# Kernel tuning notes

Measured on AMD Instinct MI355X. Metric: run time of the kernel, lower is better.

Reference implementation:

```python
import jax, jax.numpy as jnp
import numpy as np

B, S = 8, 2048

def setup_inputs() -> dict:
    key = jax.random.key(0)
    ks = iter(jax.random.split(key, 64))
    def lin(din, dout):
        w = jax.random.normal(next(ks), (din, dout), jnp.float32) / np.float32(np.sqrt(din))
        b = jax.random.normal(next(ks), (dout,), jnp.float32) * 0.01
        return w, b
    inp = {}
    inp['x'] = jax.random.normal(next(ks), (B, S, 256), jnp.float32)
    def blk(tag, d, ff):
        for name, (din, dout) in [('q',(d,d)),('k',(d,d)),('v',(d,d)),('o',(d,d)),('ff1',(d,ff)),('ff2',(ff,d))]:
            w, b = lin(din, dout)
            inp[f'{name}_w{tag}'] = w; inp[f'{name}_b{tag}'] = b
        inp[f'ln1_g{tag}'] = jnp.ones((d,), jnp.float32); inp[f'ln1_b{tag}'] = jnp.zeros((d,), jnp.float32)
        inp[f'ln2_g{tag}'] = jnp.ones((d,), jnp.float32); inp[f'ln2_b{tag}'] = jnp.zeros((d,), jnp.float32)
    blk(1, 256, 1024)
    blk(2, 128, 512)
    for nm, (din, dout) in [('dr1',(256,128)),('dr2',(128,64)),('dr3',(64,32)),('dr4',(32,14))]:
        w, b = lin(din, dout)
        inp[f'{nm}_w'] = w; inp[f'{nm}_b'] = b
    return inp

def _ln(x, g, b, eps=1e-5):
    m = x.mean(-1, keepdims=True)
    v = ((x - m) ** 2).mean(-1, keepdims=True)
    return (x - m) / jnp.sqrt(v + eps) * g + b

def _mha(x, wq, bq, wk, bk, wv, bv, wo, bo, h):
    Bx, Sx, D = x.shape
    hd = D // h
    q = (x @ wq + bq).reshape(Bx, Sx, h, hd).transpose(0, 2, 1, 3)
    k = (x @ wk + bk).reshape(Bx, Sx, h, hd).transpose(0, 2, 1, 3)
    v = (x @ wv + bv).reshape(Bx, Sx, h, hd).transpose(0, 2, 1, 3)
    scores = jnp.einsum('bhqd,bhkd->bhqk', q, k) / jnp.sqrt(jnp.float32(hd))  # [B,h,S,S]
    p = jax.nn.softmax(scores, axis=-1)
    o = jnp.einsum('bhqk,bhkd->bqhd', p, v).reshape(Bx, Sx, D)
    return o @ wo + bo

def _encoder(x, p, h):
    a = _mha(x, p['qw'], p['qb'], p['kw'], p['kb'], p['vw'], p['vb'], p['ow'], p['ob'], h)
    x = _ln(a + x, p['g1'], p['b1'])
    f = jax.nn.relu(x @ p['fw1'] + p['fb1']) @ p['fw2'] + p['fb2']
    return _ln(f + x, p['g2'], p['b2'])

def _pe(s, d):
    pos = jnp.arange(s, dtype=jnp.float32)[:, None]
    dep = jnp.arange(d, dtype=jnp.float32)[None, :]
    ang = pos / jnp.power(jnp.float32(10000.0), dep / d)
    even = (jnp.arange(d)[None, :] % 2) == 0
    return jnp.where(even, jnp.sin(ang), jnp.cos(ang))

def _forward(x,
             q_w1, q_b1, k_w1, k_b1, v_w1, v_b1, o_w1, o_b1,
             ff1_w1, ff1_b1, ff2_w1, ff2_b1, ln1_g1, ln1_b1, ln2_g1, ln2_b1,
             dr1_w, dr1_b,
             q_w2, q_b2, k_w2, k_b2, v_w2, v_b2, o_w2, o_b2,
             ff1_w2, ff1_b2, ff2_w2, ff2_b2, ln1_g2, ln1_b2, ln2_g2, ln2_b2,
             dr2_w, dr2_b, dr3_w, dr3_b, dr4_w, dr4_b):
    h = x + _pe(x.shape[1], x.shape[2])
    p1 = dict(qw=q_w1, qb=q_b1, kw=k_w1, kb=k_b1, vw=v_w1, vb=v_b1, ow=o_w1, ob=o_b1,
              fw1=ff1_w1, fb1=ff1_b1, fw2=ff2_w1, fb2=ff2_b1, g1=ln1_g1, b1=ln1_b1, g2=ln2_g1, b2=ln2_b1)
    h = _encoder(h, p1, 8)
    h = h @ dr1_w + dr1_b
    p2 = dict(qw=q_w2, qb=q_b2, kw=k_w2, kb=k_b2, vw=v_w2, vb=v_b2, ow=o_w2, ob=o_b2,
              fw1=ff1_w2, fb1=ff1_b2, fw2=ff2_w2, fb2=ff2_b2, g1=ln1_g2, b1=ln1_b2, g2=ln2_g2, b2=ln2_b2)
    h = _encoder(h, p2, 8)
    h = h @ dr2_w + dr2_b
    h = jnp.max(h, axis=1)  # AdaptiveMaxPool1d(1) over the sequence dim -> [B, 64]
    h = h @ dr3_w + dr3_b
    return h @ dr4_w + dr4_b  # [B, 14]

def reference(x,
              q_w1, q_b1, k_w1, k_b1, v_w1, v_b1, o_w1, o_b1,
              ff1_w1, ff1_b1, ff2_w1, ff2_b1, ln1_g1, ln1_b1, ln2_g1, ln2_b1,
              dr1_w, dr1_b,
              q_w2, q_b2, k_w2, k_b2, v_w2, v_b2, o_w2, o_b2,
              ff1_w2, ff1_b2, ff2_w2, ff2_b2, ln1_g2, ln1_b2, ln2_g2, ln2_b2,
              dr2_w, dr2_b, dr3_w, dr3_b, dr4_w, dr4_b):
    return _forward(x,
                    q_w1, q_b1, k_w1, k_b1, v_w1, v_b1, o_w1, o_b1,
                    ff1_w1, ff1_b1, ff2_w1, ff2_b1, ln1_g1, ln1_b1, ln2_g1, ln2_b1,
                    dr1_w, dr1_b,
                    q_w2, q_b2, k_w2, k_b2, v_w2, v_b2, o_w2, o_b2,
                    ff1_w2, ff1_b2, ff2_w2, ff2_b2, ln1_g2, ln1_b2, ln2_g2, ln2_b2,
                    dr2_w, dr2_b, dr3_w, dr3_b, dr4_w, dr4_b)
```

## Files before the change

### kernel.cpp

```cpp
#include <hip/hip_runtime.h>
#include <hip/hip_bf16.h>
#include <math.h>

#define SEQ  2048
#define BATCH 8
#define NTOK (SEQ*BATCH)

typedef __attribute__((ext_vector_type(8))) short short8v;
typedef __attribute__((ext_vector_type(4))) float f32x4;
typedef unsigned short u16;

__device__ __forceinline__ u16 f2bf(float f) {
    __hip_bfloat16 h = __float2bfloat16(f);
    return *reinterpret_cast<u16*>(&h);
}
__device__ __forceinline__ unsigned pack_bf2(float a, float b) {
    __hip_bfloat162 h = __float22bfloat162_rn(float2{a, b});
    return *reinterpret_cast<unsigned*>(&h);
}
__device__ __forceinline__ void gl_lds16(const u16* g, u16* l) {
    __builtin_amdgcn_global_load_lds(
        (const __attribute__((address_space(1))) unsigned int*)g,
        (__attribute__((address_space(3))) unsigned int*)l, 16, 0, 0);
}

struct WDescs {
    const float* src[14];
    int K[14];
    int N[14];
    long dst[14];
    float scale[14];
    int tstart[15];
};

__global__ __launch_bounds__(256) void convert_w_kernel(WDescs d, u16* __restrict__ WA) {
    __shared__ float tile[64][65];
    int blk = blockIdx.x;
    int di = 0;
    while (di < 13 && blk >= d.tstart[di + 1]) ++di;
    int t  = blk - d.tstart[di];
    int K  = d.K[di], N = d.N[di];
    int tn = N >> 6;
    int k0 = (t / tn) << 6, n0 = (t % tn) << 6;
    const float* src = d.src[di];
    float sc = d.scale[di];
    int tid = threadIdx.x;
    #pragma unroll
    for (int i = 0; i < 16; ++i) {
        int id = i * 256 + tid;
        int kk = id >> 6, nn = id & 63;
        tile[kk][nn] = src[(size_t)(k0 + kk) * N + n0 + nn];
    }
    __syncthreads();
    u16* dst = WA + d.dst[di];
    #pragma unroll
    for (int i = 0; i < 16; ++i) {
        int id = i * 256 + tid;
        int nn = id >> 6, kk = id & 63;
        dst[(size_t)(n0 + nn) * K + k0 + kk] = f2bf(tile[kk][nn] * sc);
    }
}

__global__ __launch_bounds__(256) void convert_bias_kernel(
    const float* qb1, const float* kb1, const float* vb1,
    const float* qb2, const float* kb2, const float* vb2,
    const float* dr2b, float* __restrict__ BA, float qs1, float qs2)
{
    int t = blockIdx.x * 256 + threadIdx.x;
    if      (t < 256)  BA[t] = qb1[t] * qs1;
    else if (t < 512)  BA[t] = kb1[t - 256];
    else if (t < 768)  BA[t] = vb1[t - 512];
    else if (t < 896)  BA[t] = qb2[t - 768] * qs2;
    else if (t < 1024) BA[t] = kb2[t - 896];
    else if (t < 1152) BA[t] = vb2[t - 1024];
    else if (t < 1216) BA[t] = dr2b[t - 1152];
    else if (t < 1280) BA[t] = 0.f;
}

__global__ __launch_bounds__(256) void add_pe_kernel(const float* __restrict__ x,
                                                     float* __restrict__ h,
                                                     u16* __restrict__ hb) {
    int idx = blockIdx.x * 256 + threadIdx.x;
    int s = idx >> 8;
    int d = idx & 255;
    float inv = exp2f((float)d * -0.0519051264732f);
    float ang = (float)s * inv;
    float pe  = (d & 1) ? __cosf(ang) : __sinf(ang);
    #pragma unroll
    for (int b = 0; b < BATCH; ++b) {
        size_t g = ((size_t)(b * SEQ + s) << 8) + d;
        float v = x[g] + pe;
        h[g]  = v;
        hb[g] = f2bf(v);
    }
}

template<int BM, int BN, int RELU, int WF32, int WBF16>
__global__ __launch_bounds__(256) void gemm_bf16_kernel(
    const u16* __restrict__ A, const u16* __restrict__ Bt,
    const float* __restrict__ bias, float* __restrict__ Cf,
    u16* __restrict__ Cb, int N, int K)
{
    constexpr int NMF = BM / 32;
    constexpr int NBF = BN / 32;
    __shared__ u16 As[BM * 64];
    __shared__ u16 Bs[BN * 64];
    const int tid  = threadIdx.x;
    const int lane = tid & 63;
    const int c    = lane & 15, g = lane >> 4;
    const int w    = tid >> 6;
    const int wr   = w >> 1, wc = w & 1;
    const size_t bm = (size_t)blockIdx.y * BM;
    const size_t bn = (size_t)blockIdx.x * BN;

    f32x4 acc[NMF][NBF];
    #pragma unroll
    for (int i = 0; i < NMF; ++i)
        #pragma unroll
        for (int j = 0; j < NBF; ++j) acc[i][j] = (f32x4){0.f, 0.f, 0.f, 0.f};

    const int nt = K >> 6;
    for (int t = 0; t < nt; ++t) {
        #pragma unroll
        for (int j = 0; j < BM / 32; ++j) {
            int cid = j * 256 + tid;
            int row = cid >> 3, blk = cid & 7;
            int sof = (blk ^ (row & 7)) * 8;
            gl_lds16(&A[(bm + row) * K + t * 64 + sof], &As[cid * 8]);
        }
        #pragma unroll
        for (int j = 0; j < BN / 32; ++j) {
            int cid = j * 256 + tid;
            int row = cid >> 3, blk = cid & 7;
            int sof = (blk ^ (row & 7)) * 8;
            gl_lds16(&Bt[(bn + row) * K + t * 64 + sof], &Bs[cid * 8]);
        }
        __syncthreads();
        #pragma unroll
        for (int ks2 = 0; ks2 < 2; ++ks2) {
            short8v af[NMF], bfr[NBF];
            #pragma unroll
            for (int am = 0; am < NMF; ++am) {
                int r = wr * (BM / 2) + am * 16 + c;
                af[am] = *(const short8v*)&As[r * 64 + (((ks2 * 4 + g) ^ (r & 7)) * 8)];
            }
            #pragma unroll
            for (int bn_ = 0; bn_ < NBF; ++bn_) {
                int r = wc * (BN / 2) + bn_ * 16 + c;
                bfr[bn_] = *(const short8v*)&Bs[r * 64 + (((ks2 * 4 + g) ^ (r & 7)) * 8)];
            }
            #pragma unroll
            for (int am = 0; am < NMF; ++am)
                #pragma unroll
                for (int bn_ = 0; bn_ < NBF; ++bn_)
                    acc[am][bn_] = __builtin_amdgcn_mfma_f32_16x16x32_bf16(
                                       af[am], bfr[bn_], acc[am][bn_], 0, 0, 0);
        }
        __syncthreads();
    }

    float bv[NBF];
    #pragma unroll
    for (int bn_ = 0; bn_ < NBF; ++bn_) bv[bn_] = bias[bn + wc * (BN / 2) + bn_ * 16 + c];
    #pragma unroll
    for (int am = 0; am < NMF; ++am) {
        #pragma unroll
        for (int bn_ = 0; bn_ < NBF; ++bn_) {
            #pragma unroll
            for (int i = 0; i < 4; ++i) {
                size_t row = bm + wr * (BM / 2) + am * 16 + 4 * g + i;
                size_t col = bn + wc * (BN / 2) + bn_ * 16 + c;
                float v = acc[am][bn_][i] + bv[bn_];
                if (RELU) v = fmaxf(v, 0.f);
                if (WF32)  Cf[row * N + col] = v;
                if (WBF16) Cb[row * N + col] = f2bf(v);
            }
        }
    }
}

template<int D, int WBF>
__global__ __launch_bounds__(256) void ln_residual_kernel(
    const float* __restrict__ a, const float* __restrict__ r,
    const float* __restrict__ g, const float* __restrict__ bb,
    float* __restrict__ out, u16* __restrict__ outb)
{
    const int N = D >> 6;
    int wave = threadIdx.x >> 6;
    int lane = threadIdx.x & 63;
    size_t token = (size_t)blockIdx.x * 4 + wave;
    const float* ar = a + token * D;
    const float* rr = r + token * D;

    float xv[N];
    float s = 0.f;
    #pragma unroll
    for (int i = 0; i < N; ++i) {
        int d = lane + (i << 6);
        xv[i] = ar[d] + rr[d];
        s += xv[i];
    }
    #pragma unroll
    for (int off = 1; off < 64; off <<= 1) s += __shfl_xor(s, off);
    float mean = s * (1.0f / D);
    float vs = 0.f;
    #pragma unroll
    for (int i = 0; i < N; ++i) { float d0 = xv[i] - mean; vs += d0 * d0; }
    #pragma unroll
    for (int off = 1; off < 64; off <<= 1) vs += __shfl_xor(vs, off);
    float inv = 1.0f / sqrtf(vs * (1.0f / D) + 1e-5f);
    #pragma unroll
    for (int i = 0; i < N; ++i) {
        int d = lane + (i << 6);
        float v = (xv[i] - mean) * inv * g[d] + bb[d];
        out[token * D + d] = v;
        if (WBF) outb[token * D + d] = f2bf(v);
    }
}

template<int HD>
__global__ __launch_bounds__(512) void flash_mfma_kernel(
    const u16* __restrict__ QKV, u16* __restrict__ Og, const u16* __restrict__ zsrc)
{
    constexpr int D   = 8 * HD;
    constexpr int SD  = 3 * D;
    constexpr int NDH = HD / 16;

    __shared__ u16 Ks[2][64 * 32];
    __shared__ u16 Vt[2][NDH * 16 * 64];
    __shared__ u16 Pb[128 * 64];

    const int tid  = threadIdx.x;
    const int w    = tid >> 6;
    const int lane = tid & 63;
    const int c    = lane & 15;
    const int g    = lane >> 4;

    const int H    = blockIdx.x + (blockIdx.y << 4);
    const int bh   = H & 63;
    const int qblk = H >> 6;
    const int b = bh >> 3, hh = bh & 7;
    const size_t qvbase = (size_t)b * SEQ * SD + (size_t)hh * HD;
    const size_t obase  = (size_t)b * SEQ * D  + (size_t)hh * HD;
    const int qbase = qblk * 128;

    short8v qf;
    if (HD == 16 && g >= 2) {
        short8v z = {0, 0, 0, 0, 0, 0, 0, 0};
        qf = z;
    } else {
        int qrow = qbase + w * 16 + c;
        qf = *(const short8v*)&QKV[qvbase + (size_t)qrow * SD + 8 * g];
    }

    f32x4 oacc[NDH];
    float lreg[4];
    #pragma unroll
    for (int dh = 0; dh < NDH; ++dh) oacc[dh] = (f32x4){0.f, 0.f, 0.f, 0.f};
    #pragma unroll
    for (int i = 0; i < 4; ++i) lreg[i] = 0.f;

    const bool kstager = (tid < 256);
    const int krow = tid >> 2;
    const int klb  = (tid & 3) ^ ((krow >> 1) & 3);
    const bool kzero = (HD == 16) && (klb >= 2);

    const int vtid = tid - 256;
    const int skey = vtid >> 2;
    const int sch  = (vtid & 3) * 8;
    const bool vstager = (tid >= 256) && (HD == 32 || sch < 16);
    const int spos  = ((skey >> 5) << 5) + 2 * (skey & 15) + ((skey >> 4) & 1);
    const int squad = spos >> 3, soff = spos & 7;
    const int vkc = (c & 7) ^ ((c & 8) >> 1);

    if (kstager)
        gl_lds16(kzero ? zsrc : &QKV[qvbase + (size_t)krow * SD + D + klb * 8],
                 &Ks[0][tid * 8]);
    if (vstager) {
        short8v v0 = *(const short8v*)&QKV[qvbase + (size_t)skey * SD + 2 * D + sch];
        #pragma unroll
        for (int i = 0; i < 8; ++i) {
            int row = sch + i;
            int vk = (row & 7) ^ ((row & 8) >> 1);
            Vt[0][row * 64 + ((squad ^ vk) << 3) + soff] = (u16)v0[i];
        }
    }
    __syncthreads();

    const int NT = SEQ / 64;

    auto tile_body = [&](const int buf, const int t) {
        short8v vv = {0, 0, 0, 0, 0, 0, 0, 0};
        const bool pre = (t + 1 < NT);
        if (pre) {
            if (kstager)
                gl_lds16(kzero ? zsrc
                               : &QKV[qvbase + (size_t)((t + 1) * 64 + krow) * SD + D + klb * 8],
                         &Ks[buf ^ 1][tid * 8]);
            if (vstager)
                vv = *(const short8v*)&QKV[qvbase + (size_t)((t + 1) * 64 + skey) * SD + 2 * D + sch];
        }

        short8v kf[4];
        #pragma unroll
        for (int kh = 0; kh < 4; ++kh) {
            int row = 16 * kh + c;
            kf[kh] = *(const short8v*)&Ks[buf][row * 32 + ((g ^ ((c >> 1) & 3)) * 8)];
        }
        short8v vfr[NDH][2];
        #pragma unroll
        for (int dh = 0; dh < NDH; ++dh) {
            vfr[dh][0] = *(const short8v*)&Vt[buf][(16 * dh + c) * 64 + ((g ^ vkc) << 3)];
            vfr[dh][1] = *(const short8v*)&Vt[buf][(16 * dh + c) * 64 + (((4 + g) ^ vkc) << 3)];
        }

        f32x4 s[4];
        #pragma unroll
        for (int kh = 0; kh < 4; ++kh)
            s[kh] = __builtin_amdgcn_mfma_f32_16x16x32_bf16(
                        qf, kf[kh], (f32x4){0.f, 0.f, 0.f, 0.f}, 0, 0, 0);

        #pragma unroll
        for (int i = 0; i < 4; ++i) {
            float p0 = exp2f(s[0][i]);
            float p1 = exp2f(s[1][i]);
            float p2 = exp2f(s[2][i]);
            float p3 = exp2f(s[3][i]);
            lreg[i] += (p0 + p1) + (p2 + p3);
            int rr = 4 * g + i;
            int pk = (rr & 7) ^ ((rr & 8) >> 1);
            int base = (w * 16 + rr) * 64 + 2 * (c & 3);
            *(unsigned*)&Pb[base + (((c >> 2) ^ pk) << 3)]       = pack_bf2(p0, p1);
            *(unsigned*)&Pb[base + ((((c >> 2) + 4) ^ pk) << 3)] = pack_bf2(p2, p3);
        }

        short8v pf0 = *(const short8v*)&Pb[(w * 16 + c) * 64 + ((g ^ vkc) << 3)];
        short8v pf1 = *(const short8v*)&Pb[(w * 16 + c) * 64 + (((4 + g) ^ vkc) << 3)];
        #pragma unroll
        for (int dh = 0; dh < NDH; ++dh) {
            oacc[dh] = __builtin_amdgcn_mfma_f32_16x16x32_bf16(pf0, vfr[dh][0], oacc[dh], 0, 0, 0);
            oacc[dh] = __builtin_amdgcn_mfma_f32_16x16x32_bf16(pf1, vfr[dh][1], oacc[dh], 0, 0, 0);
        }

        if (pre && vstager) {
            #pragma unroll
            for (int i = 0; i < 8; ++i) {
                int row = sch + i;
                int vk = (row & 7) ^ ((row & 8) >> 1);
                Vt[buf ^ 1][row * 64 + ((squad ^ vk) << 3) + soff] = (u16)vv[i];
            }
        }
        __syncthreads();
    };

    for (int t = 0; t < NT; t += 2) {
        tile_body(0, t);
        tile_body(1, t + 1);
    }

    #pragma unroll
    for (int i = 0; i < 4; ++i) {
        float li = lreg[i];
        li += __shfl_xor(li, 1);
        li += __shfl_xor(li, 2);
        li += __shfl_xor(li, 4);
        li += __shfl_xor(li, 8);
        float inv = 1.0f / li;
        int qrow = qbase + w * 16 + 4 * g + i;
        #pragma unroll
        for (int dh = 0; dh < NDH; ++dh)
            Og[obase + (size_t)qrow * D + 16 * dh + c] = f2bf(oacc[dh][i] * inv);
    }
}

__global__ __launch_bounds__(256) void maxpool_kernel(const float* __restrict__ in,
                                                      float* __restrict__ out) {
    __shared__ float red[4][64];
    int b = blockIdx.x, d = threadIdx.x & 63, st = threadIdx.x >> 6;
    float m = -INFINITY;
    for (int s = st * (SEQ / 4); s < (st + 1) * (SEQ / 4); ++s)
        m = fmaxf(m, in[((size_t)b * SEQ + s) * 128 + d]);
    red[st][d] = m;
    __syncthreads();
    if (st == 0) {
        m = fmaxf(fmaxf(red[0][d], red[1][d]), fmaxf(red[2][d], red[3][d]));
        out[b * 64 + d] = m;
    }
}

__global__ __launch_bounds__(256) void head_kernel(
    const float* __restrict__ pooled,
    const float* __restrict__ w3, const float* __restrict__ b3,
    const float* __restrict__ w4, const float* __restrict__ b4,
    float* __restrict__ out)
{
    __shared__ float t[8][32];
    int tid = threadIdx.x;
    {
        int b = tid >> 5, j = tid & 31;
        float s = b3[j];
        #pragma unroll
        for (int k = 0; k < 64; ++k) s = fmaf(pooled[b * 64 + k], w3[k * 32 + j], s);
        t[b][j] = s;
    }
    __syncthreads();
    if (tid < 8 * 14) {
        int b = tid / 14, j = tid % 14;
        float s = b4[j];
        #pragma unroll
        for (int k = 0; k < 32; ++k) s = fmaf(t[b][k], w4[k * 14 + j], s);
        out[b * 14 + j] = s;
    }
}

extern "C" void kernel_launch(void* const* d_in, const int* in_sizes, int n_in,
                              void* d_out, int out_size, void* d_ws, size_t ws_size,
                              hipStream_t stream) {
    const float* x     = (const float*)d_in[0];
    const float* qw1   = (const float*)d_in[1];
    const float* qb1   = (const float*)d_in[2];
    const float* kw1   = (const float*)d_in[3];
    const float* kb1   = (const float*)d_in[4];
    const float* vw1   = (const float*)d_in[5];
    const float* vb1   = (const float*)d_in[6];
    const float* ow1   = (const float*)d_in[7];
    const float* ob1   = (const float*)d_in[8];
    const float* f1w1  = (const float*)d_in[9];
    const float* f1b1  = (const float*)d_in[10];
    const float* f2w1  = (const float*)d_in[11];
    const float* f2b1  = (const float*)d_in[12];
    const float* ln1g1 = (const float*)d_in[13];
    const float* ln1b1 = (const float*)d_in[14];
    const float* ln2g1 = (const float*)d_in[15];
    const float* ln2b1 = (const float*)d_in[16];
    const float* qw2   = (const float*)d_in[17];
    const float* qb2   = (const float*)d_in[18];
    const float* kw2   = (const float*)d_in[19];
    const float* kb2   = (const float*)d_in[20];
    const float* vw2   = (const float*)d_in[21];
    const float* vb2   = (const float*)d_in[22];
    const float* ow2   = (const float*)d_in[23];
    const float* ob2   = (const float*)d_in[24];
    const float* f1w2  = (const float*)d_in[25];
    const float* f1b2  = (const float*)d_in[26];
    const float* f2w2  = (const float*)d_in[27];
    const float* f2b2  = (const float*)d_in[28];
    const float* ln1g2 = (const float*)d_in[29];
    const float* ln1b2 = (const float*)d_in[30];
    const float* ln2g2 = (const float*)d_in[31];
    const float* ln2b2 = (const float*)d_in[32];
    const float* dr1w  = (const float*)d_in[33];
    const float* dr1b  = (const float*)d_in[34];
    const float* dr2w  = (const float*)d_in[35];
    const float* dr2b  = (const float*)d_in[36];
    const float* dr3w  = (const float*)d_in[37];
    const float* dr3b  = (const float*)d_in[38];
    const float* dr4w  = (const float*)d_in[39];
    const float* dr4b  = (const float*)d_in[40];

    const size_t T = NTOK;
    float* F1 = (float*)d_ws;
    float* F2 = F1 + T * 256;
    u16*   E1 = (u16*)(F2 + T * 256);
    u16*   E2 = E1 + T * 256;
    u16*   E3 = E2 + T * 256;
    u16*   Dq = E3 + T * 256;
    u16*   WA = Dq + T * 1024;
    float* BA = (float*)(WA + 1048576);
    const u16* ZS = (const u16*)(BA + 1216);

    const float QS1 = 0.25503488f;
    const float QS2 = 0.36067376f;

    WDescs wd;
    const float* srcs[14] = {qw1, kw1, vw1, ow1, f1w1, f2w1, dr1w,
                             qw2, kw2, vw2, ow2, f1w2, f2w2, dr2w};
    int Ks_[14]  = {256, 256, 256, 256, 256, 1024, 256, 128, 128, 128, 128, 128, 512, 128};
    int Ns_[14]  = {256, 256, 256, 256, 1024, 256, 128, 128, 128, 128, 128, 512, 128, 64};
    long dsts[14] = {0, 65536, 131072, 196608, 262144, 524288, 786432,
                     819200, 835584, 851968, 868352, 884736, 950272, 1015808};
    float scs[14] = {QS1, 1.f, 1.f, 1.f, 1.f, 1.f, 1.f, QS2, 1.f, 1.f, 1.f, 1.f, 1.f, 1.f};
    int tst[15] = {0, 16, 32, 48, 64, 128, 192, 200, 204, 208, 212, 216, 232, 248, 250};
    for (int i = 0; i < 14; ++i) {
        wd.src[i] = srcs[i]; wd.K[i] = Ks_[i]; wd.N[i] = Ns_[i];
        wd.dst[i] = dsts[i]; wd.scale[i] = scs[i];
    }
    for (int i = 0; i < 15; ++i) wd.tstart[i] = tst[i];

    const dim3 blk(256);
    const dim3 blk512(512);

    convert_w_kernel<<<250, blk, 0, stream>>>(wd, WA);
    convert_bias_kernel<<<5, blk, 0, stream>>>(qb1, kb1, vb1, qb2, kb2, vb2, dr2b, BA, QS1, QS2);

    add_pe_kernel<<<SEQ, blk, 0, stream>>>(x, F1, E1);

    gemm_bf16_kernel<128,128,0,0,1><<<dim3(6, 128), blk, 0, stream>>>(E1, WA + 0,      BA,   nullptr, Dq, 768, 256);
    flash_mfma_kernel<32><<<dim3(16, 64), blk512, 0, stream>>>(Dq, E2, ZS);
    gemm_bf16_kernel< 64, 64,0,1,0><<<dim3(4, 256), blk, 0, stream>>>(E2, WA + 196608, ob1,  F2, nullptr, 256, 256);
    ln_residual_kernel<256,1><<<NTOK / 4, blk, 0, stream>>>(F2, F1, ln1g1, ln1b1, F1, E1);
    gemm_bf16_kernel<128,128,1,0,1><<<dim3(8, 128), blk, 0, stream>>>(E1, WA + 262144, f1b1, nullptr, Dq, 1024, 256);
    gemm_bf16_kernel< 64, 64,0,1,0><<<dim3(4, 256), blk, 0, stream>>>(Dq, WA + 524288, f2b1, F2, nullptr, 256, 1024);
    ln_residual_kernel<256,1><<<NTOK / 4, blk, 0, stream>>>(F2, F1, ln2g1, ln2b1, F1, E1);

    gemm_bf16_kernel< 64, 64,0,1,1><<<dim3(2, 256), blk, 0, stream>>>(E1, WA + 786432, dr1b, F2, E2, 128, 256);

    gemm_bf16_kernel< 64, 64,0,0,1><<<dim3(6, 256), blk, 0, stream>>>(E2, WA + 819200, BA + 768, nullptr, Dq, 384, 128);
    flash_mfma_kernel<16><<<dim3(16, 64), blk512, 0, stream>>>(Dq, E3, ZS);
    gemm_bf16_kernel< 64, 64,0,1,0><<<dim3(2, 256), blk, 0, stream>>>(E3, WA + 868352, ob2,  F1, nullptr, 128, 128);
    ln_residual_kernel<128,1><<<NTOK / 4, blk, 0, stream>>>(F1, F2, ln1g2, ln1b2, F2, E1);
    gemm_bf16_kernel< 64, 64,1,0,1><<<dim3(8, 256), blk, 0, stream>>>(E1, WA + 884736, f1b2, nullptr, Dq, 512, 128);
    gemm_bf16_kernel< 64, 64,0,1,0><<<dim3(2, 256), blk, 0, stream>>>(Dq, WA + 950272, f2b2, F1, nullptr, 128, 512);
    ln_residual_kernel<128,1><<<NTOK / 4, blk, 0, stream>>>(F1, F2, ln2g2, ln2b2, F2, E1);

    gemm_bf16_kernel< 64, 64,0,1,0><<<dim3(2, 256), blk, 0, stream>>>(E1, WA + 1015808, BA + 1152, F1, nullptr, 128, 128);
    maxpool_kernel<<<BATCH, blk, 0, stream>>>(F1, F2);
    head_kernel<<<1, blk, 0, stream>>>(F2, dr3w, dr3b, dr4w, dr4b, (float*)d_out);
}
```

Measured before the change: 585.8 us.

## Double-buffer GEMM, emit bf16 pre-LN outputs, fuse maxpool into final GEMM

The GEMM kernel gets double-buffered LDS staging with a fixed 64-row tile, and the launches are retuned to new grid shapes. Pre-LayerNorm GEMMs now write bf16 instead of fp32, and the LN kernel reads bf16 and skips its fp32 output when nothing needs it. The final dr2 GEMM computes per-block column maxima in its epilogue, head_kernel reduces those partials, and the separate maxpool kernel is removed. s_setprio hints are added around the MFMA sections in flash attention. These changes cut memory traffic and kernel launches, at the cost of more LDS per GEMM block and bf16 rounding of the residual inputs to LN.

```diff
diff --git a/kernel.cpp b/kernel.cpp
--- a/kernel.cpp
+++ b/kernel.cpp
@@ -13,6 +13,10 @@
 __device__ __forceinline__ u16 f2bf(float f) {
     __hip_bfloat16 h = __float2bfloat16(f);
     return *reinterpret_cast<u16*>(&h);
+}
+__device__ __forceinline__ float bf2f(u16 u) {
+    unsigned v = ((unsigned)u) << 16;
+    return *reinterpret_cast<float*>(&v);
 }
 __device__ __forceinline__ unsigned pack_bf2(float a, float b) {
     __hip_bfloat162 h = __float22bfloat162_rn(float2{a, b});
@@ -95,16 +99,17 @@
     }
 }
 
-template<int BM, int BN, int RELU, int WF32, int WBF16>
+template<int BN, int RELU, int WF32, int WBF16, int MAXEP>
 __global__ __launch_bounds__(256) void gemm_bf16_kernel(
     const u16* __restrict__ A, const u16* __restrict__ Bt,
     const float* __restrict__ bias, float* __restrict__ Cf,
-    u16* __restrict__ Cb, int N, int K)
+    u16* __restrict__ Cb, float* __restrict__ Pm, int N, int K)
 {
-    constexpr int NMF = BM / 32;
+    constexpr int BM  = 64;
+    constexpr int NMF = 2;
     constexpr int NBF = BN / 32;
-    __shared__ u16 As[BM * 64];
-    __shared__ u16 Bs[BN * 64];
+    __shared__ u16 As[2][BM * 64];
+    __shared__ u16 Bs[2][BN * 64];
     const int tid  = threadIdx.x;
     const int lane = tid & 63;
     const int c    = lane & 15, g = lane >> 4;
@@ -119,35 +124,41 @@
         #pragma unroll
         for (int j = 0; j < NBF; ++j) acc[i][j] = (f32x4){0.f, 0.f, 0.f, 0.f};
 
-    const int nt = K >> 6;
-    for (int t = 0; t < nt; ++t) {
+    auto stage = [&](int buf, int t) {
         #pragma unroll
         for (int j = 0; j < BM / 32; ++j) {
             int cid = j * 256 + tid;
             int row = cid >> 3, blk = cid & 7;
             int sof = (blk ^ (row & 7)) * 8;
-            gl_lds16(&A[(bm + row) * K + t * 64 + sof], &As[cid * 8]);
+            gl_lds16(&A[(bm + row) * K + t * 64 + sof], &As[buf][cid * 8]);
         }
         #pragma unroll
         for (int j = 0; j < BN / 32; ++j) {
             int cid = j * 256 + tid;
             int row = cid >> 3, blk = cid & 7;
             int sof = (blk ^ (row & 7)) * 8;
-            gl_lds16(&Bt[(bn + row) * K + t * 64 + sof], &Bs[cid * 8]);
-        }
-        __syncthreads();
+            gl_lds16(&Bt[(bn + row) * K + t * 64 + sof], &Bs[buf][cid * 8]);
+        }
+    };
+
+    const int nt = K >> 6;
+    stage(0, 0);
+    __syncthreads();
+    for (int t = 0; t < nt; ++t) {
+        if (t + 1 < nt) stage((t + 1) & 1, t + 1);
+        const int bfi = t & 1;
         #pragma unroll
         for (int ks2 = 0; ks2 < 2; ++ks2) {
             short8v af[NMF], bfr[NBF];
             #pragma unroll
             for (int am = 0; am < NMF; ++am) {
-                int r = wr * (BM / 2) + am * 16 + c;
-                af[am] = *(const short8v*)&As[r * 64 + (((ks2 * 4 + g) ^ (r & 7)) * 8)];
+                int r = wr * 32 + am * 16 + c;
+                af[am] = *(const short8v*)&As[bfi][r * 64 + (((ks2 * 4 + g) ^ (r & 7)) * 8)];
             }
             #pragma unroll
             for (int bn_ = 0; bn_ < NBF; ++bn_) {
                 int r = wc * (BN / 2) + bn_ * 16 + c;
-                bfr[bn_] = *(const short8v*)&Bs[r * 64 + (((ks2 * 4 + g) ^ (r & 7)) * 8)];
+                bfr[bn_] = *(const short8v*)&Bs[bfi][r * 64 + (((ks2 * 4 + g) ^ (r & 7)) * 8)];
             }
             #pragma unroll
             for (int am = 0; am < NMF; ++am)
@@ -162,13 +173,36 @@
     float bv[NBF];
     #pragma unroll
     for (int bn_ = 0; bn_ < NBF; ++bn_) bv[bn_] = bias[bn + wc * (BN / 2) + bn_ * 16 + c];
+
+    if (MAXEP) {
+        __shared__ float cm[8][64];
+        #pragma unroll
+        for (int bn_ = 0; bn_ < NBF; ++bn_) {
+            float lm = -INFINITY;
+            #pragma unroll
+            for (int am = 0; am < NMF; ++am)
+                #pragma unroll
+                for (int i = 0; i < 4; ++i)
+                    lm = fmaxf(lm, acc[am][bn_][i] + bv[bn_]);
+            cm[wr * 4 + g][wc * (BN / 2) + bn_ * 16 + c] = lm;
+        }
+        __syncthreads();
+        if (tid < 64) {
+            float m = cm[0][tid];
+            #pragma unroll
+            for (int k = 1; k < 8; ++k) m = fmaxf(m, cm[k][tid]);
+            Pm[(size_t)blockIdx.y * 64 + tid] = m;
+        }
+        return;
+    }
+
     #pragma unroll
     for (int am = 0; am < NMF; ++am) {
         #pragma unroll
         for (int bn_ = 0; bn_ < NBF; ++bn_) {
             #pragma unroll
             for (int i = 0; i < 4; ++i) {
-                size_t row = bm + wr * (BM / 2) + am * 16 + 4 * g + i;
+                size_t row = bm + wr * 32 + am * 16 + 4 * g + i;
                 size_t col = bn + wc * (BN / 2) + bn_ * 16 + c;
                 float v = acc[am][bn_][i] + bv[bn_];
                 if (RELU) v = fmaxf(v, 0.f);
@@ -179,9 +213,9 @@
     }
 }
 
-template<int D, int WBF>
+template<int D, int WRF>
 __global__ __launch_bounds__(256) void ln_residual_kernel(
-    const float* __restrict__ a, const float* __restrict__ r,
+    const u16* __restrict__ a, const float* __restrict__ r,
     const float* __restrict__ g, const float* __restrict__ bb,
     float* __restrict__ out, u16* __restrict__ outb)
 {
@@ -189,7 +223,7 @@
     int wave = threadIdx.x >> 6;
     int lane = threadIdx.x & 63;
     size_t token = (size_t)blockIdx.x * 4 + wave;
-    const float* ar = a + token * D;
+    const u16*   ar = a + token * D;
     const float* rr = r + token * D;
 
     float xv[N];
@@ -197,7 +231,7 @@
     #pragma unroll
     for (int i = 0; i < N; ++i) {
         int d = lane + (i << 6);
-        xv[i] = ar[d] + rr[d];
+        xv[i] = bf2f(ar[d]) + rr[d];
         s += xv[i];
     }
     #pragma unroll
@@ -213,8 +247,8 @@
     for (int i = 0; i < N; ++i) {
         int d = lane + (i << 6);
         float v = (xv[i] - mean) * inv * g[d] + bb[d];
-        out[token * D + d] = v;
-        if (WBF) outb[token * D + d] = f2bf(v);
+        if (WRF) out[token * D + d] = v;
+        outb[token * D + d] = f2bf(v);
     }
 }
 
@@ -315,10 +349,12 @@
         }
 
         f32x4 s[4];
+        __builtin_amdgcn_s_setprio(1);
         #pragma unroll
         for (int kh = 0; kh < 4; ++kh)
             s[kh] = __builtin_amdgcn_mfma_f32_16x16x32_bf16(
                         qf, kf[kh], (f32x4){0.f, 0.f, 0.f, 0.f}, 0, 0, 0);
+        __builtin_amdgcn_s_setprio(0);
 
         #pragma unroll
         for (int i = 0; i < 4; ++i) {
@@ -336,11 +372,13 @@
 
         short8v pf0 = *(const short8v*)&Pb[(w * 16 + c) * 64 + ((g ^ vkc) << 3)];
         short8v pf1 = *(const short8v*)&Pb[(w * 16 + c) * 64 + (((4 + g) ^ vkc) << 3)];
+        __builtin_amdgcn_s_setprio(1);
         #pragma unroll
         for (int dh = 0; dh < NDH; ++dh) {
             oacc[dh] = __builtin_amdgcn_mfma_f32_16x16x32_bf16(pf0, vfr[dh][0], oacc[dh], 0, 0, 0);
             oacc[dh] = __builtin_amdgcn_mfma_f32_16x16x32_bf16(pf1, vfr[dh][1], oacc[dh], 0, 0, 0);
         }
+        __builtin_amdgcn_s_setprio(0);
 
         if (pre && vstager) {
             #pragma unroll
@@ -373,42 +411,39 @@
     }
 }
 
-__global__ __launch_bounds__(256) void maxpool_kernel(const float* __restrict__ in,
-                                                      float* __restrict__ out) {
-    __shared__ float red[4][64];
-    int b = blockIdx.x, d = threadIdx.x & 63, st = threadIdx.x >> 6;
-    float m = -INFINITY;
-    for (int s = st * (SEQ / 4); s < (st + 1) * (SEQ / 4); ++s)
-        m = fmaxf(m, in[((size_t)b * SEQ + s) * 128 + d]);
-    red[st][d] = m;
-    __syncthreads();
-    if (st == 0) {
-        m = fmaxf(fmaxf(red[0][d], red[1][d]), fmaxf(red[2][d], red[3][d]));
-        out[b * 64 + d] = m;
-    }
-}
-
 __global__ __launch_bounds__(256) void head_kernel(
-    const float* __restrict__ pooled,
+    const float* __restrict__ Pm,
     const float* __restrict__ w3, const float* __restrict__ b3,
     const float* __restrict__ w4, const float* __restrict__ b4,
     float* __restrict__ out)
 {
-    __shared__ float t[8][32];
+    __shared__ float pooled[8][64];
+    __shared__ float t2[8][32];
     int tid = threadIdx.x;
+    #pragma unroll
+    for (int rep = 0; rep < 2; ++rep) {
+        int idx = rep * 256 + tid;
+        int b = idx >> 6, d = idx & 63;
+        float m = -INFINITY;
+        #pragma unroll
+        for (int k = 0; k < 32; ++k)
+            m = fmaxf(m, Pm[(size_t)(b * 32 + k) * 64 + d]);
+        pooled[b][d] = m;
+    }
+    __syncthreads();
     {
         int b = tid >> 5, j = tid & 31;
         float s = b3[j];
         #pragma unroll
-        for (int k = 0; k < 64; ++k) s = fmaf(pooled[b * 64 + k], w3[k * 32 + j], s);
-        t[b][j] = s;
+        for (int k = 0; k < 64; ++k) s = fmaf(pooled[b][k], w3[k * 32 + j], s);
+        t2[b][j] = s;
     }
     __syncthreads();
     if (tid < 8 * 14) {
         int b = tid / 14, j = tid % 14;
         float s = b4[j];
         #pragma unroll
-        for (int k = 0; k < 32; ++k) s = fmaf(t[b][k], w4[k * 14 + j], s);
+        for (int k = 0; k < 32; ++k) s = fmaf(t2[b][k], w4[k * 14 + j], s);
         out[b * 14 + j] = s;
     }
 }
@@ -495,25 +530,24 @@
 
     add_pe_kernel<<<SEQ, blk, 0, stream>>>(x, F1, E1);
 
-    gemm_bf16_kernel<128,128,0,0,1><<<dim3(6, 128), blk, 0, stream>>>(E1, WA + 0,      BA,   nullptr, Dq, 768, 256);
+    gemm_bf16_kernel<128,0,0,1,0><<<dim3(6, 256), blk, 0, stream>>>(E1, WA + 0,      BA,   nullptr, Dq, nullptr, 768, 256);
     flash_mfma_kernel<32><<<dim3(16, 64), blk512, 0, stream>>>(Dq, E2, ZS);
-    gemm_bf16_kernel< 64, 64,0,1,0><<<dim3(4, 256), blk, 0, stream>>>(E2, WA + 196608, ob1,  F2, nullptr, 256, 256);
-    ln_residual_kernel<256,1><<<NTOK / 4, blk, 0, stream>>>(F2, F1, ln1g1, ln1b1, F1, E1);
-    gemm_bf16_kernel<128,128,1,0,1><<<dim3(8, 128), blk, 0, stream>>>(E1, WA + 262144, f1b1, nullptr, Dq, 1024, 256);
-    gemm_bf16_kernel< 64, 64,0,1,0><<<dim3(4, 256), blk, 0, stream>>>(Dq, WA + 524288, f2b1, F2, nullptr, 256, 1024);
-    ln_residual_kernel<256,1><<<NTOK / 4, blk, 0, stream>>>(F2, F1, ln2g1, ln2b1, F1, E1);
-
-    gemm_bf16_kernel< 64, 64,0,1,1><<<dim3(2, 256), blk, 0, stream>>>(E1, WA + 786432, dr1b, F2, E2, 128, 256);
-
-    gemm_bf16_kernel< 64, 64,0,0,1><<<dim3(6, 256), blk, 0, stream>>>(E2, WA + 819200, BA + 768, nullptr, Dq, 384, 128);
+    gemm_bf16_kernel< 64,0,0,1,0><<<dim3(4, 256), blk, 0, stream>>>(E2, WA + 196608, ob1,  nullptr, E3, nullptr, 256, 256);
+    ln_residual_kernel<256,1><<<NTOK / 4, blk, 0, stream>>>(E3, F1, ln1g1, ln1b1, F1, E1);
+    gemm_bf16_kernel<128,1,0,1,0><<<dim3(8, 256), blk, 0, stream>>>(E1, WA + 262144, f1b1, nullptr, Dq, nullptr, 1024, 256);
+    gemm_bf16_kernel< 64,0,0,1,0><<<dim3(4, 256), blk, 0, stream>>>(Dq, WA + 524288, f2b1, nullptr, E3, nullptr, 256, 1024);
+    ln_residual_kernel<256,1><<<NTOK / 4, blk, 0, stream>>>(E3, F1, ln2g1, ln2b1, F1, E1);
+
+    gemm_bf16_kernel< 64,0,1,1,0><<<dim3(2, 256), blk, 0, stream>>>(E1, WA + 786432, dr1b, F2, E2, nullptr, 128, 256);
+
+    gemm_bf16_kernel<128,0,0,1,0><<<dim3(3, 256), blk, 0, stream>>>(E2, WA + 819200, BA + 768, nullptr, Dq, nullptr, 384, 128);
     flash_mfma_kernel<16><<<dim3(16, 64), blk512, 0, stream>>>(Dq, E3, ZS);
-    gemm_bf16_kernel< 64, 64,0,1,0><<<dim3(2, 256), blk, 0, stream>>>(E3, WA + 868352, ob2,  F1, nullptr, 128, 128);
-    ln_residual_kernel<128,1><<<NTOK / 4, blk, 0, stream>>>(F1, F2, ln1g2, ln1b2, F2, E1);
-    gemm_bf16_kernel< 64, 64,1,0,1><<<dim3(8, 256), blk, 0, stream>>>(E1, WA + 884736, f1b2, nullptr, Dq, 512, 128);
-    gemm_bf16_kernel< 64, 64,0,1,0><<<dim3(2, 256), blk, 0, stream>>>(Dq, WA + 950272, f2b2, F1, nullptr, 128, 512);
-    ln_residual_kernel<128,1><<<NTOK / 4, blk, 0, stream>>>(F1, F2, ln2g2, ln2b2, F2, E1);
-
-    gemm_bf16_kernel< 64, 64,0,1,0><<<dim3(2, 256), blk, 0, stream>>>(E1, WA + 1015808, BA + 1152, F1, nullptr, 128, 128);
-    maxpool_kernel<<<BATCH, blk, 0, stream>>>(F1, F2);
-    head_kernel<<<1, blk, 0, stream>>>(F2, dr3w, dr3b, dr4w, dr4b, (float*)d_out);
-}
+    gemm_bf16_kernel< 64,0,0,1,0><<<dim3(2, 256), blk, 0, stream>>>(E3, WA + 868352, ob2,  nullptr, E2, nullptr, 128, 128);
+    ln_residual_kernel<128,1><<<NTOK / 4, blk, 0, stream>>>(E2, F2, ln1g2, ln1b2, F2, E1);
+    gemm_bf16_kernel<128,1,0,1,0><<<dim3(4, 256), blk, 0, stream>>>(E1, WA + 884736, f1b2, nullptr, Dq, nullptr, 512, 128);
+    gemm_bf16_kernel< 64,0,0,1,0><<<dim3(2, 256), blk, 0, stream>>>(Dq, WA + 950272, f2b2, nullptr, E2, nullptr, 128, 512);
+    ln_residual_kernel<128,0><<<NTOK / 4, blk, 0, stream>>>(E2, F2, ln2g2, ln2b2, nullptr, E1);
+
+    gemm_bf16_kernel< 64,0,0,0,1><<<dim3(1, 256), blk, 0, stream>>>(E1, WA + 1015808, BA + 1152, nullptr, nullptr, F1, 64, 128);
+    head_kernel<<<1, blk, 0, stream>>>(F1, dr3w, dr3b, dr4w, dr4b, (float*)d_out);
+}
```

Result: faster. 489.9 us (-16.4%).
